# Optimization experiments

Measured on AMD Instinct MI355X. Metric: run time of the kernel, lower is better.

Reference implementation:

```python
import jax, jax.numpy as jnp
import numpy as np

N_NODES = 50000
N_EDGES = 600000
DIM = 128


def setup_inputs() -> dict:
    key = jax.random.key(0)
    k1, k2, k3, k4, k5, k6 = jax.random.split(key, 6)
    return {
        "h_v": jax.random.normal(k1, (N_NODES, DIM), dtype=jnp.float32),
        "h_d": jax.random.normal(k2, (N_EDGES, DIM), dtype=jnp.float32),
        "W_pi": jax.random.normal(k3, (DIM, 1), dtype=jnp.float32) * (1.0 / np.sqrt(DIM)),
        "W_M": jax.random.normal(k4, (2 * DIM, 1), dtype=jnp.float32) * (1.0 / np.sqrt(2 * DIM)),
        "src": jax.random.randint(k5, (N_EDGES,), 0, N_NODES, dtype=jnp.int64) if jax.config.jax_enable_x64 else jax.random.randint(k5, (N_EDGES,), 0, N_NODES, dtype=jnp.int32),
        "dst": jax.random.randint(k6, (N_EDGES,), 0, N_NODES, dtype=jnp.int32),
    }


def reference(h_v, h_d, W_pi, W_M, src, dst):
    # Gather per-edge endpoint features: [E, dim]
    ft_s = h_v[src]
    ft_d = h_v[dst]
    prod = ft_s * ft_d                                   # u_mul_v
    # e = pi(src*dst*d): [E, 1]
    e = (prod * h_d) @ W_pi
    # mask = sigmoid(M(cat([src*dst, d]))): [E, 1]
    mask = jax.nn.sigmoid(jnp.concatenate([prod, h_d], axis=-1) @ W_M)
    logits = (e * mask)[:, 0]                            # [E]
    # edge_softmax grouped by destination node (DGL semantics)
    seg_max = jax.ops.segment_max(logits, dst, num_segments=N_NODES)
    ex = jnp.exp(logits - seg_max[dst])
    seg_sum = jax.ops.segment_sum(ex, dst, num_segments=N_NODES)
    a = ex / seg_sum[dst]                                # [E]
    # dropout_local is identity at inference
    # message m = ft_src * a; aggregate sum over incoming edges per dst node
    out = jax.ops.segment_sum(ft_s * a[:, None], dst, num_segments=N_NODES)
    return out
```

## Files before the change

### kernel.cpp

```cpp
#include <hip/hip_runtime.h>

#define NN 50000
#define NE 600000
#define DIM 128
#define NB 196


__global__ __launch_bounds__(256) void zero_counts_kernel(int* __restrict__ counts) {
    int i = blockIdx.x * 256 + threadIdx.x;
    if (i < NN) counts[i] = 0;
}

__global__ __launch_bounds__(256) void hist_kernel(const int* __restrict__ dst,
                                                   int* __restrict__ counts) {
    int e = blockIdx.x * 256 + threadIdx.x;
    if (e < NE) atomicAdd(&counts[dst[e]], 1);
}

__global__ __launch_bounds__(256) void scan_pass1_kernel(const int* __restrict__ counts,
                                                         int* __restrict__ offsets,
                                                         int* __restrict__ blockSums) {
    __shared__ int tmp[256];
    int tid = threadIdx.x;
    int i = blockIdx.x * 256 + tid;
    int v = (i < NN) ? counts[i] : 0;
    tmp[tid] = v;
    __syncthreads();
    #pragma unroll
    for (int off = 1; off < 256; off <<= 1) {
        int t = (tid >= off) ? tmp[tid - off] : 0;
        __syncthreads();
        tmp[tid] += t;
        __syncthreads();
    }
    int incl = tmp[tid];
    if (i < NN) offsets[i] = incl - v;
    if (tid == 255) blockSums[blockIdx.x] = incl;
}

__global__ __launch_bounds__(256) void scan_pass2_kernel(int* __restrict__ blockSums) {
    __shared__ int tmp[256];
    int tid = threadIdx.x;
    int v = (tid < NB) ? blockSums[tid] : 0;
    tmp[tid] = v;
    __syncthreads();
    #pragma unroll
    for (int off = 1; off < 256; off <<= 1) {
        int t = (tid >= off) ? tmp[tid - off] : 0;
        __syncthreads();
        tmp[tid] += t;
        __syncthreads();
    }
    if (tid < NB) blockSums[tid] = tmp[tid] - v;
}

__global__ __launch_bounds__(256) void scan_pass3_kernel(int* __restrict__ offsets,
                                                         const int* __restrict__ blockSums,
                                                         int* __restrict__ cursor) {
    int i = blockIdx.x * 256 + threadIdx.x;
    if (i < NN) {
        int o = offsets[i] + blockSums[i >> 8];
        offsets[i] = o;
        cursor[i] = o;
    }
    if (i == 0) offsets[NN] = NE;
}


__global__ __launch_bounds__(256) void edge_logits_fused_kernel(
    const float* __restrict__ h_v, const float* __restrict__ h_d,
    const float* __restrict__ W_pi, const float* __restrict__ W_M,
    const int* __restrict__ src, const int* __restrict__ dst,
    int* __restrict__ cursor,
    int* __restrict__ src_sorted, float* __restrict__ logit_sorted) {
    int idx = blockIdx.x * 256 + threadIdx.x;
    int e = idx >> 5;
    int lane32 = threadIdx.x & 31;
    if (e >= NE) return;
    int s = src[e];
    int d = dst[e];
    const float4 fs = ((const float4*)(h_v + (size_t)s * DIM))[lane32];
    const float4 fd = ((const float4*)(h_v + (size_t)d * DIM))[lane32];
    const float4 hd = ((const float4*)(h_d + (size_t)e * DIM))[lane32];
    const float4 wp = ((const float4*)W_pi)[lane32];
    const float4 m0 = ((const float4*)W_M)[lane32];
    const float4 m1 = ((const float4*)(W_M + DIM))[lane32];

    float px = fs.x * fd.x, py = fs.y * fd.y, pz = fs.z * fd.z, pw = fs.w * fd.w;
    float s1 = px * hd.x * wp.x + py * hd.y * wp.y + pz * hd.z * wp.z + pw * hd.w * wp.w;
    float s2 = px * m0.x + py * m0.y + pz * m0.z + pw * m0.w
             + hd.x * m1.x + hd.y * m1.y + hd.z * m1.z + hd.w * m1.w;

    #pragma unroll
    for (int off = 16; off > 0; off >>= 1) {
        s1 += __shfl_xor(s1, off, 64);
        s2 += __shfl_xor(s2, off, 64);
    }
    if (lane32 == 0) {
        float logit = s1 / (1.0f + __expf(-s2));
        int pos = atomicAdd(&cursor[d], 1);
        src_sorted[pos] = s;
        logit_sorted[pos] = logit;
    }
}


__global__ __launch_bounds__(256) void node_aggregate_kernel(
    const float* __restrict__ h_v,
    const int* __restrict__ offsets,
    const int* __restrict__ src_sorted, const float* __restrict__ logit_sorted,
    float* __restrict__ out) {
    int node = (blockIdx.x * 256 + threadIdx.x) >> 6;
    int lane = threadIdx.x & 63;
    if (node >= NN) return;
    int beg = offsets[node];
    int end = offsets[node + 1];

    float mx = -__builtin_inff();
    for (int k = beg + lane; k < end; k += 64) mx = fmaxf(mx, logit_sorted[k]);
    #pragma unroll
    for (int off = 32; off > 0; off >>= 1) mx = fmaxf(mx, __shfl_xor(mx, off, 64));

    float2 acc = make_float2(0.0f, 0.0f);
    float ssum = 0.0f;
    for (int k = beg; k < end; ++k) {
        float lg = logit_sorted[k];
        int s = src_sorted[k];
        float ex = __expf(lg - mx);
        ssum += ex;
        const float2 v = ((const float2*)(h_v + (size_t)s * DIM))[lane];
        acc.x += v.x * ex;
        acc.y += v.y * ex;
    }
    float inv = (ssum > 0.0f) ? 1.0f / ssum : 0.0f;
    ((float2*)(out + (size_t)node * DIM))[lane] = make_float2(acc.x * inv, acc.y * inv);
}


extern "C" void kernel_launch(void* const* d_in, const int* in_sizes, int n_in,
                              void* d_out, int out_size, void* d_ws, size_t ws_size,
                              hipStream_t stream) {
    const float* h_v  = (const float*)d_in[0];
    const float* h_d  = (const float*)d_in[1];
    const float* W_pi = (const float*)d_in[2];
    const float* W_M  = (const float*)d_in[3];
    const int*   src  = (const int*)d_in[4];
    const int*   dst  = (const int*)d_in[5];
    float* out = (float*)d_out;

    int* counts        = (int*)d_ws;
    int* offsets       = counts + NN;
    int* cursor        = offsets + NN + 1;
    int* blockSums     = cursor + NN;
    int* src_sorted    = blockSums + 256;
    float* logit_sorted = (float*)(src_sorted + NE);

    zero_counts_kernel<<<NB, 256, 0, stream>>>(counts);
    hist_kernel<<<(NE + 255) / 256, 256, 0, stream>>>(dst, counts);
    scan_pass1_kernel<<<NB, 256, 0, stream>>>(counts, offsets, blockSums);
    scan_pass2_kernel<<<1, 256, 0, stream>>>(blockSums);
    scan_pass3_kernel<<<NB, 256, 0, stream>>>(offsets, blockSums, cursor);
    edge_logits_fused_kernel<<<(NE * 32 + 255) / 256, 256, 0, stream>>>(
        h_v, h_d, W_pi, W_M, src, dst, cursor, src_sorted, logit_sorted);
    node_aggregate_kernel<<<(NN * 64 + 255) / 256, 256, 0, stream>>>(
        h_v, offsets, src_sorted, logit_sorted, out);
}
```

Measured before the change: 587.4 us.

## Precompute exp in edge kernel, pack src/weight pairs, split aggregate into half-waves

```diff
diff --git a/kernel.cpp b/kernel.cpp
--- a/kernel.cpp
+++ b/kernel.cpp
@@ -71,8 +71,7 @@
     const float* __restrict__ h_v, const float* __restrict__ h_d,
     const float* __restrict__ W_pi, const float* __restrict__ W_M,
     const int* __restrict__ src, const int* __restrict__ dst,
-    int* __restrict__ cursor,
-    int* __restrict__ src_sorted, float* __restrict__ logit_sorted) {
+    int* __restrict__ cursor, float2* __restrict__ pairs) {
     int idx = blockIdx.x * 256 + threadIdx.x;
     int e = idx >> 5;
     int lane32 = threadIdx.x & 31;
@@ -98,9 +97,9 @@
     }
     if (lane32 == 0) {
         float logit = s1 / (1.0f + __expf(-s2));
+        float ex = __expf(logit);
         int pos = atomicAdd(&cursor[d], 1);
-        src_sorted[pos] = s;
-        logit_sorted[pos] = logit;
+        pairs[pos] = make_float2(__int_as_float(s), ex);
     }
 }
 
@@ -108,32 +107,40 @@
 __global__ __launch_bounds__(256) void node_aggregate_kernel(
     const float* __restrict__ h_v,
     const int* __restrict__ offsets,
-    const int* __restrict__ src_sorted, const float* __restrict__ logit_sorted,
+    const float2* __restrict__ pairs,
     float* __restrict__ out) {
     int node = (blockIdx.x * 256 + threadIdx.x) >> 6;
     int lane = threadIdx.x & 63;
     if (node >= NN) return;
+    int half = lane >> 5;
+    int l32 = lane & 31;
     int beg = offsets[node];
     int end = offsets[node + 1];
 
-    float mx = -__builtin_inff();
-    for (int k = beg + lane; k < end; k += 64) mx = fmaxf(mx, logit_sorted[k]);
-    #pragma unroll
-    for (int off = 32; off > 0; off >>= 1) mx = fmaxf(mx, __shfl_xor(mx, off, 64));
-
-    float2 acc = make_float2(0.0f, 0.0f);
+    float4 acc = make_float4(0.0f, 0.0f, 0.0f, 0.0f);
     float ssum = 0.0f;
-    for (int k = beg; k < end; ++k) {
-        float lg = logit_sorted[k];
-        int s = src_sorted[k];
-        float ex = __expf(lg - mx);
-        ssum += ex;
-        const float2 v = ((const float2*)(h_v + (size_t)s * DIM))[lane];
+    for (int k = beg + half; k < end; k += 2) {
+        float2 p = pairs[k];
+        int s = __float_as_int(p.x);
+        float ex = p.y;
+        const float4 v = ((const float4*)(h_v + (size_t)s * DIM))[l32];
         acc.x += v.x * ex;
         acc.y += v.y * ex;
+        acc.z += v.z * ex;
+        acc.w += v.w * ex;
+        ssum += ex;
     }
-    float inv = (ssum > 0.0f) ? 1.0f / ssum : 0.0f;
-    ((float2*)(out + (size_t)node * DIM))[lane] = make_float2(acc.x * inv, acc.y * inv);
+    acc.x += __shfl_xor(acc.x, 32, 64);
+    acc.y += __shfl_xor(acc.y, 32, 64);
+    acc.z += __shfl_xor(acc.z, 32, 64);
+    acc.w += __shfl_xor(acc.w, 32, 64);
+    ssum  += __shfl_xor(ssum, 32, 64);
+
+    if (half == 0) {
+        float inv = (ssum > 0.0f) ? 1.0f / ssum : 0.0f;
+        ((float4*)(out + (size_t)node * DIM))[l32] =
+            make_float4(acc.x * inv, acc.y * inv, acc.z * inv, acc.w * inv);
+    }
 }
 
 
@@ -148,12 +155,11 @@
     const int*   dst  = (const int*)d_in[5];
     float* out = (float*)d_out;
 
-    int* counts        = (int*)d_ws;
-    int* offsets       = counts + NN;
-    int* cursor        = offsets + NN + 1;
-    int* blockSums     = cursor + NN;
-    int* src_sorted    = blockSums + 256;
-    float* logit_sorted = (float*)(src_sorted + NE);
+    int* counts     = (int*)d_ws;
+    int* offsets    = counts + NN;
+    int* cursor     = offsets + NN + 1;
+    int* blockSums  = cursor + NN;
+    float2* pairs   = (float2*)(((uintptr_t)(blockSums + 256) + 7) & ~(uintptr_t)7);
 
     zero_counts_kernel<<<NB, 256, 0, stream>>>(counts);
     hist_kernel<<<(NE + 255) / 256, 256, 0, stream>>>(dst, counts);
@@ -161,7 +167,7 @@
     scan_pass2_kernel<<<1, 256, 0, stream>>>(blockSums);
     scan_pass3_kernel<<<NB, 256, 0, stream>>>(offsets, blockSums, cursor);
     edge_logits_fused_kernel<<<(NE * 32 + 255) / 256, 256, 0, stream>>>(
-        h_v, h_d, W_pi, W_M, src, dst, cursor, src_sorted, logit_sorted);
+        h_v, h_d, W_pi, W_M, src, dst, cursor, pairs);
     node_aggregate_kernel<<<(NN * 64 + 255) / 256, 256, 0, stream>>>(
-        h_v, offsets, src_sorted, logit_sorted, out);
+        h_v, offsets, pairs, out);
 }
```

After: 557.5 us. 1.05x faster.
